# Kernel tuning notes

Measured on AMD Instinct MI355X. Metric: run time of the kernel, lower is better.

## Reference

```python
import jax, jax.numpy as jnp
import numpy as np

B, S, D, H = 2, 2048, 1024, 16
DH = D // H  # 64


def setup_inputs() -> dict:
    key = jax.random.key(0)
    ks = jax.random.split(key, 12)
    inp = {
        "hidden_states": jax.random.normal(ks[0], (B, S, D), dtype=jnp.float32),
        "attention_mask": jax.random.randint(ks[1], (B, S), 0, 2, dtype=jnp.int32),
        "Wq": jax.random.normal(ks[2], (D, D), dtype=jnp.float32) / np.sqrt(D),
        "bq": jnp.zeros((D,), dtype=jnp.float32),
        "Wk": jax.random.normal(ks[3], (D, D), dtype=jnp.float32) / np.sqrt(D),
        "bk": jnp.zeros((D,), dtype=jnp.float32),
        "Wv": jax.random.normal(ks[4], (D, D), dtype=jnp.float32) / np.sqrt(D),
        "bv": jnp.zeros((D,), dtype=jnp.float32),
        # per-head additive query bias (emotion manipulation path)
        "emotion_w": jax.random.normal(ks[5], (H, DH), dtype=jnp.float32),
        "Wo": jax.random.normal(ks[6], (D, D), dtype=jnp.float32) / np.sqrt(D),
        "bo": jnp.zeros((D,), dtype=jnp.float32),
    }
    return inp


def reference(hidden_states, attention_mask, Wq, bq, Wk, bk, Wv, bv, emotion_w, Wo, bo):
    b, s, d = hidden_states.shape
    # projections -> [b, h, s, dh]
    def proj(W, bias):
        y = hidden_states @ W + bias
        return y.reshape(b, s, H, DH).transpose(0, 2, 1, 3)

    q = proj(Wq, bq)
    k = proj(Wk, bk)
    v = proj(Wv, bv)

    # manipulation_type='emotion': additive per-head query bias
    q = q + emotion_w[None, :, None, :]

    scores = jnp.einsum("bhqd,bhkd->bhqk", q, k) / np.sqrt(DH).astype(np.float32)
    # key-padding mask: positions where mask==0 get -inf
    scores = jnp.where(attention_mask[:, None, None, :] == 0, -jnp.inf, scores)
    attn = jax.nn.softmax(scores, axis=-1)  # dropout is identity in eval mode

    out = jnp.einsum("bhqk,bhkd->bhqd", attn, v)
    out = out.transpose(0, 2, 1, 3).reshape(b, s, d)
    return out @ Wo + bo
```

## Files before the change

kernel.cpp:

```cpp
#include <hip/hip_runtime.h>
#include <hip/hip_bf16.h>


#define B_  2
#define S_  2048
#define D_  1024
#define K_  1024
#define H_  16
#define DH_ 64
#define BS_ (B_*S_)

typedef __hip_bfloat16 bf16;
typedef __attribute__((ext_vector_type(8))) short s8v;
typedef __attribute__((ext_vector_type(4))) short s4v;
typedef __attribute__((ext_vector_type(4))) float f4v;

__device__ __forceinline__ float b2f(bf16 x) { return __bfloat162float(x); }
__device__ __forceinline__ bf16  f2b(float x) { return __float2bfloat16(x); }

__device__ __forceinline__ void gl_lds_16B(const bf16* g, bf16* l) {
    __builtin_amdgcn_global_load_lds(
        (const __attribute__((address_space(1))) unsigned int*)g,
        (__attribute__((address_space(3))) unsigned int*)l, 16, 0, 0);
}

#define QSCALE_ 0.1803368801f

__global__ __launch_bounds__(256) void prep_kernel(
    const float* __restrict__ X, const int* __restrict__ mask,
    const float* __restrict__ Wq, const float* __restrict__ Wk,
    const float* __restrict__ Wv, const float* __restrict__ Wo,
    bf16* __restrict__ Xb, bf16* __restrict__ mkbf,
    bf16* __restrict__ WTq, bf16* __restrict__ WTk,
    bf16* __restrict__ WTv, bf16* __restrict__ WTo)
{
    __shared__ float Ls[64][68];
    const int blk = blockIdx.x;
    const int t   = threadIdx.x;

    if (blk < 1024) {
        const int z   = blk >> 8;
        const int t16 = blk & 255;
        const int k0  = (t16 >> 4) * 64;
        const int n0  = (t16 & 15) * 64;
        const float* __restrict__ W = (z == 0) ? Wq : (z == 1) ? Wk : (z == 2) ? Wv : Wo;
        bf16* __restrict__ WT       = (z == 0) ? WTq : (z == 1) ? WTk : (z == 2) ? WTv : WTo;

        const int lr = t >> 4;
        const int lc = (t & 15) * 4;
        #pragma unroll
        for (int i = 0; i < 4; i++) {
            const int k = i * 16 + lr;
            const float4 v = *(const float4*)(W + (size_t)(k0 + k) * K_ + n0 + lc);
            Ls[k][lc + 0] = v.x; Ls[k][lc + 1] = v.y;
            Ls[k][lc + 2] = v.z; Ls[k][lc + 3] = v.w;
        }
        __syncthreads();
        #pragma unroll
        for (int i = 0; i < 4; i++) {
            const int n = i * 16 + lr;
            s4v o;
            #pragma unroll
            for (int j = 0; j < 4; j++) {
                bf16 tb = f2b(Ls[lc + j][n]);
                o[j] = *(short*)&tb;
            }
            *(s4v*)(WT + (size_t)(n0 + n) * K_ + k0 + lc) = o;
        }
    } else if (blk < 5120) {
        const size_t idx = ((size_t)(blk - 1024) * 256 + t) * 4;
        const float4 v = *(const float4*)(X + idx);
        bf16 t0 = f2b(v.x), t1 = f2b(v.y), t2 = f2b(v.z), t3 = f2b(v.w);
        s4v o;
        o[0] = *(short*)&t0; o[1] = *(short*)&t1;
        o[2] = *(short*)&t2; o[3] = *(short*)&t3;
        *(s4v*)(Xb + idx) = o;
    } else {
        const int idx = (blk - 5120) * 256 + t;
        mkbf[idx] = f2b(mask[idx] ? 1.0f : 0.0f);
    }
}

template <bool SWAPPED>
__device__ __forceinline__ void gemm_tile(
    const bf16* __restrict__ A, const bf16* __restrict__ BT,
    int m0, int n0, bf16* As, bf16* Bs, f4v acc[4][4])
{
    const int t    = threadIdx.x;
    const int lane = t & 63;
    const int wave = t >> 6;
    const int quad = lane >> 4;
    const int l15  = lane & 15;
    const int wr   = wave >> 1;
    const int wc   = wave & 1;

    const int sr = t >> 3;
    const int sc = (t & 7) * 8;

    for (int kb = 0; kb < K_; kb += 64) {
        #pragma unroll
        for (int i = 0; i < 4; i++) {
            const int r = i * 32 + sr;
            gl_lds_16B(A  + (size_t)(m0 + r) * K_ + kb + sc, As + r * 64 + sc);
            gl_lds_16B(BT + (size_t)(n0 + r) * K_ + kb + sc, Bs + r * 64 + sc);
        }
        __syncthreads();

        #pragma unroll
        for (int ks = 0; ks < 2; ks++) {
            s8v fA[4], fB[4];
            #pragma unroll
            for (int i = 0; i < 4; i++) {
                fA[i] = *(const s8v*)&As[(wr * 64 + i * 16 + l15) * 64 + ks * 32 + quad * 8];
                fB[i] = *(const s8v*)&Bs[(wc * 64 + i * 16 + l15) * 64 + ks * 32 + quad * 8];
            }
            #pragma unroll
            for (int i = 0; i < 4; i++)
                #pragma unroll
                for (int j = 0; j < 4; j++)
                    acc[i][j] = SWAPPED
                        ? __builtin_amdgcn_mfma_f32_16x16x32_bf16(fB[i], fA[j], acc[i][j], 0, 0, 0)
                        : __builtin_amdgcn_mfma_f32_16x16x32_bf16(fA[i], fB[j], acc[i][j], 0, 0, 0);
        }
        __syncthreads();
    }
}

__global__ __launch_bounds__(256) void proj_qkv_kernel(
    const bf16* __restrict__ Xb,
    const bf16* __restrict__ WTq, const float* __restrict__ bq,
    const bf16* __restrict__ WTk, const float* __restrict__ bk,
    const bf16* __restrict__ WTv, const float* __restrict__ bv,
    const float* __restrict__ emo, const int* __restrict__ mask,
    bf16* __restrict__ q_ws, bf16* __restrict__ k_ws, bf16* __restrict__ v_ws)
{
    const int m0 = blockIdx.x * 128;
    const int n0 = blockIdx.y * 128;
    const int z  = blockIdx.z;

    __shared__ __align__(16) bf16 As[128 * 64];
    __shared__ __align__(16) bf16 Bs[128 * 64];

    const int t    = threadIdx.x;
    const int lane = t & 63;
    const int wave = t >> 6;
    const int quad = lane >> 4;
    const int l15  = lane & 15;
    const int wr   = wave >> 1;
    const int wc   = wave & 1;

    f4v acc[4][4] = {};

    if (z == 0) {
        gemm_tile<false>(Xb, WTq, m0, n0, As, Bs, acc);
        #pragma unroll
        for (int j = 0; j < 4; j++) {
            const int n  = n0 + wc * 64 + j * 16 + l15;
            const int h  = n >> 6, dh = n & 63;
            const float bias_n = bq[n] + emo[n];
            #pragma unroll
            for (int i = 0; i < 4; i++) {
                #pragma unroll
                for (int r = 0; r < 4; r++) {
                    const int m = m0 + wr * 64 + i * 16 + quad * 4 + r;
                    const int b = m >> 11, s = m & 2047;
                    q_ws[(((size_t)(b * H_ + h)) * S_ + s) * DH_ + dh] =
                        f2b((acc[i][j][r] + bias_n) * QSCALE_);
                }
            }
        }
    } else if (z == 1) {
        gemm_tile<false>(Xb, WTk, m0, n0, As, Bs, acc);
        #pragma unroll
        for (int j = 0; j < 4; j++) {
            const int n  = n0 + wc * 64 + j * 16 + l15;
            const int h  = n >> 6, dh = n & 63;
            const float bias_n = bk[n];
            #pragma unroll
            for (int i = 0; i < 4; i++) {
                #pragma unroll
                for (int r = 0; r < 4; r++) {
                    const int m = m0 + wr * 64 + i * 16 + quad * 4 + r;
                    const int b = m >> 11, s = m & 2047;
                    k_ws[(((size_t)(b * H_ + h)) * S_ + s) * DH_ + dh] =
                        f2b(acc[i][j][r] + bias_n);
                }
            }
        }
    } else {
        gemm_tile<true>(Xb, WTv, m0, n0, As, Bs, acc);
        #pragma unroll
        for (int j = 0; j < 4; j++) {
            const int m = m0 + wr * 64 + j * 16 + l15;
            const int b = m >> 11, s = m & 2047;
            const float msk = mask[b * S_ + s] ? 1.0f : 0.0f;
            #pragma unroll
            for (int i = 0; i < 4; i++) {
                #pragma unroll
                for (int r = 0; r < 4; r++) {
                    const int n  = n0 + wc * 64 + i * 16 + quad * 4 + r;
                    const int h  = n >> 6, dh = n & 63;
                    v_ws[(((size_t)(b * H_ + h)) * DH_ + dh) * S_ + s] =
                        f2b((acc[i][j][r] + bv[n]) * msk);
                }
            }
        }
    }
}

__global__ __launch_bounds__(256) void proj_out_kernel(
    const bf16* __restrict__ ctx, const bf16* __restrict__ WTo,
    const float* __restrict__ bo, float* __restrict__ out)
{
    const int m0 = blockIdx.x * 128;
    const int n0 = blockIdx.y * 128;

    __shared__ __align__(16) bf16 As[128 * 64];
    __shared__ __align__(16) bf16 Bs[128 * 64];

    const int t    = threadIdx.x;
    const int lane = t & 63;
    const int wave = t >> 6;
    const int quad = lane >> 4;
    const int l15  = lane & 15;
    const int wr   = wave >> 1;
    const int wc   = wave & 1;

    f4v acc[4][4] = {};
    gemm_tile<false>(ctx, WTo, m0, n0, As, Bs, acc);

    #pragma unroll
    for (int j = 0; j < 4; j++) {
        const int n = n0 + wc * 64 + j * 16 + l15;
        const float bias_n = bo[n];
        #pragma unroll
        for (int i = 0; i < 4; i++) {
            #pragma unroll
            for (int r = 0; r < 4; r++) {
                const int m = m0 + wr * 64 + i * 16 + quad * 4 + r;
                out[(size_t)m * D_ + n] = acc[i][j][r] + bias_n;
            }
        }
    }
}

#define PP_ 88

__global__ __launch_bounds__(256) void attn_kernel(
    const bf16* __restrict__ q_ws, const bf16* __restrict__ k_ws,
    const bf16* __restrict__ v_ws, const bf16* __restrict__ mkbf,
    bf16* __restrict__ ctx)
{
    const int bh = blockIdx.x;
    const int q0 = blockIdx.y * 128;
    const int b  = bh >> 4;
    const int h  = bh & 15;

    __shared__ __align__(16) bf16 k_lds[64 * 64];
    __shared__ __align__(16) bf16 vt_lds[64 * 64];
    __shared__ __align__(16) bf16 p_lds[4][32 * PP_];

    const int t    = threadIdx.x;
    const int wave = t >> 6;
    const int lane = t & 63;
    const int quad = lane >> 4;
    const int l15  = lane & 15;
    const int lxor = l15 & 7;

    s8v qf[2][2];
    #pragma unroll
    for (int qs = 0; qs < 2; qs++)
        #pragma unroll
        for (int dt = 0; dt < 2; dt++)
            qf[qs][dt] = *(const s8v*)(q_ws +
                ((size_t)bh * S_ + q0 + wave * 32 + qs * 16 + l15) * DH_ + dt * 32 + quad * 8);

    f4v oacc[2][4] = {};
    f4v osum[2]    = {};

    int srw[2], scs[2];
    #pragma unroll
    for (int c = 0; c < 2; c++) {
        const int e = c * 2048 + t * 8;
        srw[c] = e >> 6;
        scs[c] = ((e >> 3) & 7) ^ (srw[c] & 7);
    }

    for (int kb0 = 0; kb0 < S_; kb0 += 64) {
        #pragma unroll
        for (int c = 0; c < 2; c++) {
            const int e = c * 2048 + t * 8;
            const int r = srw[c], cs = scs[c];
            gl_lds_16B(k_ws + ((size_t)bh * S_ + kb0) * DH_ + r * 64 + cs * 8,
                       k_lds + e);
            gl_lds_16B(v_ws + ((size_t)bh * DH_ + r) * S_ + kb0 + cs * 8,
                       vt_lds + e);
        }
        __syncthreads();

        f4v sacc[2][4] = {};
        #pragma unroll
        for (int kt = 0; kt < 4; kt++) {
            #pragma unroll
            for (int dt = 0; dt < 2; dt++) {
                const s8v kf = *(const s8v*)&k_lds[(kt * 16 + l15) * 64 +
                                                   ((dt * 4 + quad) ^ lxor) * 8];
                #pragma unroll
                for (int qs = 0; qs < 2; qs++)
                    sacc[qs][kt] = __builtin_amdgcn_mfma_f32_16x16x32_bf16(kf, qf[qs][dt], sacc[qs][kt], 0, 0, 0);
            }
        }

        #pragma unroll
        for (int qs = 0; qs < 2; qs++) {
            #pragma unroll
            for (int kt = 0; kt < 4; kt++) {
                float2 e01, e23;
                e01.x = exp2f(sacc[qs][kt][0]);
                e01.y = exp2f(sacc[qs][kt][1]);
                e23.x = exp2f(sacc[qs][kt][2]);
                e23.y = exp2f(sacc[qs][kt][3]);
                union { __hip_bfloat162 hh; unsigned u; } lo, hi;
                lo.hh = __float22bfloat162_rn(e01);
                hi.hh = __float22bfloat162_rn(e23);
                *(uint2*)&p_lds[wave][(qs * 16 + l15) * PP_ + kt * 16 + quad * 4] =
                    make_uint2(lo.u, hi.u);
            }
        }

        __builtin_amdgcn_s_waitcnt(0xC07F);

        #pragma unroll
        for (int kh = 0; kh < 2; kh++) {
            s8v ap[2];
            #pragma unroll
            for (int qs = 0; qs < 2; qs++)
                ap[qs] = *(const s8v*)&p_lds[wave][(qs * 16 + l15) * PP_ + kh * 32 + quad * 8];
            const s8v mv = *(const s8v*)(mkbf + (size_t)b * S_ + kb0 + kh * 32 + quad * 8);
            #pragma unroll
            for (int nt = 0; nt < 4; nt++) {
                const s8v vf = *(const s8v*)&vt_lds[(nt * 16 + l15) * 64 +
                                                    ((kh * 4 + quad) ^ lxor) * 8];
                #pragma unroll
                for (int qs = 0; qs < 2; qs++)
                    oacc[qs][nt] = __builtin_amdgcn_mfma_f32_16x16x32_bf16(ap[qs], vf, oacc[qs][nt], 0, 0, 0);
            }
            #pragma unroll
            for (int qs = 0; qs < 2; qs++)
                osum[qs] = __builtin_amdgcn_mfma_f32_16x16x32_bf16(ap[qs], mv, osum[qs], 0, 0, 0);
        }
        __syncthreads();
    }

    #pragma unroll
    for (int qs = 0; qs < 2; qs++) {
        #pragma unroll
        for (int r = 0; r < 4; r++) {
            const float inv = 1.0f / osum[qs][r];
            const int q = q0 + wave * 32 + qs * 16 + quad * 4 + r;
            #pragma unroll
            for (int nt = 0; nt < 4; nt++)
                ctx[((size_t)b * S_ + q) * D_ + h * DH_ + nt * 16 + l15] =
                    f2b(oacc[qs][nt][r] * inv);
        }
    }
}

extern "C" void kernel_launch(void* const* d_in, const int* in_sizes, int n_in,
                              void* d_out, int out_size, void* d_ws, size_t ws_size,
                              hipStream_t stream) {
    (void)in_sizes; (void)n_in; (void)out_size; (void)ws_size;

    const float* X    = (const float*)d_in[0];
    const int*   mask = (const int*)d_in[1];
    const float* Wq   = (const float*)d_in[2];
    const float* bq   = (const float*)d_in[3];
    const float* Wk   = (const float*)d_in[4];
    const float* bk   = (const float*)d_in[5];
    const float* Wv   = (const float*)d_in[6];
    const float* bv   = (const float*)d_in[7];
    const float* emo  = (const float*)d_in[8];
    const float* Wo   = (const float*)d_in[9];
    const float* bo   = (const float*)d_in[10];
    float* out = (float*)d_out;

    bf16* q_ws = (bf16*)d_ws;
    bf16* k_ws = q_ws + (size_t)BS_ * D_;
    bf16* v_ws = k_ws + (size_t)BS_ * D_;
    bf16* ctx  = v_ws + (size_t)BS_ * D_;
    bf16* Xb   = ctx  + (size_t)BS_ * D_;
    bf16* WTq  = Xb   + (size_t)BS_ * D_;
    bf16* WTk  = WTq  + (size_t)D_ * K_;
    bf16* WTv  = WTk  + (size_t)D_ * K_;
    bf16* WTo  = WTv  + (size_t)D_ * K_;
    bf16* mkbf = WTo  + (size_t)D_ * K_;

    hipLaunchKernelGGL(prep_kernel, dim3(5136), dim3(256), 0, stream,
                       X, mask, Wq, Wk, Wv, Wo, Xb, mkbf, WTq, WTk, WTv, WTo);
    hipLaunchKernelGGL(proj_qkv_kernel, dim3(BS_ / 128, D_ / 128, 3), dim3(256), 0, stream,
                       Xb, WTq, bq, WTk, bk, WTv, bv, emo, mask, q_ws, k_ws, v_ws);
    hipLaunchKernelGGL(attn_kernel, dim3(B_ * H_, S_ / 128), dim3(256), 0, stream,
                       q_ws, k_ws, v_ws, mkbf, ctx);
    hipLaunchKernelGGL(proj_out_kernel, dim3(BS_ / 128, D_ / 128), dim3(256), 0, stream,
                       ctx, WTo, bo, out);
}
```

Baseline: 232.5 us.

## Split attention over key halves and add a reduction kernel

Splits the attention key range into two halves across a new grid dimension, so twice as many blocks run (1024 instead of 512). Each half writes unnormalized bf16 partial outputs and row sums, which a new elementwise reduce kernel adds and normalizes. The partials and sums reuse the Xb and WTq workspace buffers. In exchange it adds an extra launch, extra memory traffic and bf16 rounding of the partials. This is valid without a running max only because the softmax is computed without max subtraction.

```diff
diff --git a/kernel.cpp b/kernel.cpp
--- a/kernel.cpp
+++ b/kernel.cpp
@@ -249,12 +249,15 @@
 __global__ __launch_bounds__(256) void attn_kernel(
     const bf16* __restrict__ q_ws, const bf16* __restrict__ k_ws,
     const bf16* __restrict__ v_ws, const bf16* __restrict__ mkbf,
-    bf16* __restrict__ ctx)
+    bf16* __restrict__ opart0, bf16* __restrict__ opart1,
+    float* __restrict__ osum_ws)
 {
     const int bh = blockIdx.x;
     const int q0 = blockIdx.y * 128;
+    const int z  = blockIdx.z;
     const int b  = bh >> 4;
     const int h  = bh & 15;
+    bf16* __restrict__ opart = z ? opart1 : opart0;
 
     __shared__ __align__(16) bf16 k_lds[64 * 64];
     __shared__ __align__(16) bf16 vt_lds[64 * 64];
@@ -286,7 +289,9 @@
         scs[c] = ((e >> 3) & 7) ^ (srw[c] & 7);
     }
 
-    for (int kb0 = 0; kb0 < S_; kb0 += 64) {
+    const int kbase = z * (S_ / 2);
+    for (int it = 0; it < S_ / 128; it++) {
+        const int kb0 = kbase + it * 64;
         #pragma unroll
         for (int c = 0; c < 2; c++) {
             const int e = c * 2048 + t * 8;
@@ -356,14 +361,43 @@
     for (int qs = 0; qs < 2; qs++) {
         #pragma unroll
         for (int r = 0; r < 4; r++) {
-            const float inv = 1.0f / osum[qs][r];
             const int q = q0 + wave * 32 + qs * 16 + quad * 4 + r;
+            if (l15 == 0)
+                osum_ws[((z << 5) + bh) * S_ + q] = osum[qs][r];
             #pragma unroll
             for (int nt = 0; nt < 4; nt++)
-                ctx[((size_t)b * S_ + q) * D_ + h * DH_ + nt * 16 + l15] =
-                    f2b(oacc[qs][nt][r] * inv);
-        }
-    }
+                opart[((size_t)b * S_ + q) * D_ + h * DH_ + nt * 16 + l15] =
+                    f2b(oacc[qs][nt][r]);
+        }
+    }
+}
+
+__global__ __launch_bounds__(256) void reduce_kernel(
+    const bf16* __restrict__ opart1, const float* __restrict__ osum_ws,
+    bf16* __restrict__ ctx)
+{
+    const int g = blockIdx.x * 256 + threadIdx.x;
+    const size_t f = (size_t)g * 8;
+    const int dhf = (int)(f & 1023);
+    const int h   = dhf >> 6;
+    const int s   = (int)((f >> 10) & 2047);
+    const int b   = (int)(f >> 21);
+    const int bh  = b * H_ + h;
+
+    const float l   = osum_ws[bh * S_ + s] + osum_ws[((1 << 5) + bh) * S_ + s];
+    const float inv = 1.0f / l;
+
+    const s8v a0 = *(const s8v*)(ctx + f);
+    const s8v a1 = *(const s8v*)(opart1 + f);
+    s8v o;
+    #pragma unroll
+    for (int j = 0; j < 8; j++) {
+        short s0 = a0[j], s1 = a1[j];
+        const float v = (b2f(*(bf16*)&s0) + b2f(*(bf16*)&s1)) * inv;
+        bf16 ob = f2b(v);
+        o[j] = *(short*)&ob;
+    }
+    *(s8v*)(ctx + f) = o;
 }
 
 extern "C" void kernel_launch(void* const* d_in, const int* in_sizes, int n_in,
@@ -399,8 +433,10 @@
                        X, mask, Wq, Wk, Wv, Wo, Xb, mkbf, WTq, WTk, WTv, WTo);
     hipLaunchKernelGGL(proj_qkv_kernel, dim3(BS_ / 128, D_ / 128, 3), dim3(256), 0, stream,
                        Xb, WTq, bq, WTk, bk, WTv, bv, emo, mask, q_ws, k_ws, v_ws);
-    hipLaunchKernelGGL(attn_kernel, dim3(B_ * H_, S_ / 128), dim3(256), 0, stream,
-                       q_ws, k_ws, v_ws, mkbf, ctx);
+    hipLaunchKernelGGL(attn_kernel, dim3(B_ * H_, S_ / 128, 2), dim3(256), 0, stream,
+                       q_ws, k_ws, v_ws, mkbf, ctx, Xb, (float*)WTq);
+    hipLaunchKernelGGL(reduce_kernel, dim3(BS_ * D_ / (256 * 8)), dim3(256), 0, stream,
+                       Xb, (const float*)WTq, ctx);
     hipLaunchKernelGGL(proj_out_kernel, dim3(BS_ / 128, D_ / 128), dim3(256), 0, stream,
                        ctx, WTo, bo, out);
 }
```

Measured after the change: 241.3 us. 1.04x slower.
